# Kernel optimization log

Measured on AMD Instinct MI355X. Metric: run time of the kernel, lower is better.

## Reference

```python
import jax, jax.numpy as jnp
import numpy as np

B, HEADS, T, QH, QW, D = 2, 8, 8, 16, 16, 64
KT, KH, KW = T, QH, QW  # key shape == query shape


def _rel_index(q_n, k_n):
    q_ratio = round(max(k_n / q_n, 1.0))
    k_ratio = round(max(q_n / k_n, 1.0))
    d = jnp.arange(q_n)[:, None] * q_ratio - jnp.arange(k_n)[None, :] * k_ratio
    return d + (k_n - 1) * k_ratio  # [q_n, k_n] indices into embedding table


def setup_inputs() -> dict:
    key = jax.random.key(0)
    k1, k2, k3, k4, k5 = jax.random.split(key, 5)
    query = jax.random.normal(k1, (B, HEADS, T * QH * QW, D), dtype=jnp.float32)
    scores = jax.random.normal(k2, (B, HEADS, T * QH * QW, KT * KH * KW), dtype=jnp.float32)
    height_emb = jax.random.normal(k3, (2 * (max(QH, KH) - 1) + 1, D), dtype=jnp.float32)
    width_emb = jax.random.normal(k4, (2 * (max(QW, KW) - 1) + 1, D), dtype=jnp.float32)
    time_emb = jax.random.normal(k5, (2 * (max(T, KT) - 1) + 1, D), dtype=jnp.float32)
    return {"query": query, "scores": scores, "height_emb": height_emb,
            "width_emb": width_emb, "time_emb": time_emb}


def reference(query, scores, height_emb, width_emb, time_emb):
    # gather relative-position embeddings (static indices)
    Rh = height_emb[_rel_index(QH, KH)]   # [qh, kh, D]
    Rw = width_emb[_rel_index(QW, KW)]    # [qw, kw, D]
    Rt = time_emb[_rel_index(T, KT)]      # [t,  kt, D]

    q = query.reshape(B, HEADS, T, QH, QW, D)
    rel_h = jnp.einsum('bNthwc,hkc->bNthwk', q, Rh)  # [B,N,T,qh,qw,kh]
    rel_w = jnp.einsum('bNthwc,wkc->bNthwk', q, Rw)  # [B,N,T,qh,qw,kw]
    rel_t = jnp.einsum('bNthwc,tkc->bNthwk', q, Rt)  # [B,N,T,qh,qw,kt]

    s = scores.reshape(B, HEADS, T, QH, QW, KT, KH, KW)
    s = s + rel_h[:, :, :, :, :, None, :, None]
    s = s + rel_w[:, :, :, :, :, None, None, :]
    s = s + rel_t[:, :, :, :, :, :, None, None]
    return s.reshape(B, HEADS, T * QH * QW, KT * KH * KW)
```

## Files before the change

kernel.cpp:

```cpp
#include <hip/hip_runtime.h>


__global__ __launch_bounds__(256) void relpos_fused_kernel(
    const float* __restrict__ query,
    const float* __restrict__ scores,
    const float* __restrict__ hemb,
    const float* __restrict__ wemb,
    const float* __restrict__ temb,
    float* __restrict__ out)
{
    __shared__ float q_lds[64];
    __shared__ float relH[16];
    __shared__ float relW[16];
    __shared__ float relT[8];
    __shared__ float relTH[128];

    const int bid = blockIdx.x;
    const int tid = threadIdx.x;
    const int row = bid & 2047;
    const int t   = row >> 8;
    const int qh  = (row >> 4) & 15;
    const int qw  = row & 15;

    if (tid < 16) {
        ((float4*)q_lds)[tid] =
            ((const float4*)(query + (size_t)bid * 64))[tid];
    }
    __syncthreads();

    if (tid < 40) {
        const float* emb;
        int eidx;
        if (tid < 16)      { emb = hemb; eidx = qh - tid + 15; }
        else if (tid < 32) { emb = wemb; eidx = qw - (tid - 16) + 15; }
        else               { emb = temb; eidx = t  - (tid - 32) + 7; }
        const float4* e4 = (const float4*)(emb + eidx * 64);
        const float4* q4p = (const float4*)q_lds;
        float acc = 0.f;
        #pragma unroll
        for (int k = 0; k < 16; ++k) {
            float4 q4 = q4p[k];
            float4 e  = e4[k];
            acc += q4.x * e.x + q4.y * e.y + q4.z * e.z + q4.w * e.w;
        }
        if (tid < 16)      relH[tid] = acc;
        else if (tid < 32) relW[tid - 16] = acc;
        else               relT[tid - 32] = acc;
    }
    __syncthreads();

    if (tid < 128) {
        relTH[tid] = relT[tid >> 4] + relH[tid & 15];
    }
    __syncthreads();

    const size_t base4 = (size_t)bid * 512;
    const float4* s4p = (const float4*)scores + base4;
    float4* o4p = (float4*)out + base4;
    const float4* w4p = (const float4*)relW;

    #pragma unroll
    for (int it = 0; it < 2; ++it) {
        const int j4 = tid + it * 256;
        float4 s = s4p[j4];
        const float a  = relTH[j4 >> 2];
        const float4 w = w4p[j4 & 3];
        float4 o;
        o.x = s.x + a + w.x;
        o.y = s.y + a + w.y;
        o.z = s.z + a + w.z;
        o.w = s.w + a + w.w;
        o4p[j4] = o;
    }
}

extern "C" void kernel_launch(void* const* d_in, const int* in_sizes, int n_in,
                              void* d_out, int out_size, void* d_ws, size_t ws_size,
                              hipStream_t stream) {
    const float* query  = (const float*)d_in[0];
    const float* scores = (const float*)d_in[1];
    const float* hemb   = (const float*)d_in[2];
    const float* wemb   = (const float*)d_in[3];
    const float* temb   = (const float*)d_in[4];
    float* out = (float*)d_out;

    relpos_fused_kernel<<<32768, 256, 0, stream>>>(
        query, scores, hemb, wemb, temb, out);
}
```

Measured before the change: 106.6 us.

## Process four rows per block with per-wave bias computation and nontemporal streaming

Each block now handles four query rows, with each wavefront computing its own row's 40 relative-position dot products directly from global memory. This removes the query LDS staging and the relTH pass, cutting the kernel from three barriers to one. The streaming add uses nontemporal loads and stores over 8 float4 per thread. The grid shrinks by four, which amortizes per-block setup but lowers the block count and puts more bandwidth-bound work on each thread.

```diff
diff --git a/kernel.cpp b/kernel.cpp
--- a/kernel.cpp
+++ b/kernel.cpp
@@ -1,7 +1,11 @@
 #include <hip/hip_runtime.h>
 
 
-__global__ __launch_bounds__(256) void relpos_fused_kernel(
+#define ROWS 4
+
+typedef float v4f __attribute__((ext_vector_type(4)));
+
+__global__ __launch_bounds__(256) void relpos_fused_v3(
     const float* __restrict__ query,
     const float* __restrict__ scores,
     const float* __restrict__ hemb,
@@ -9,68 +13,55 @@
     const float* __restrict__ temb,
     float* __restrict__ out)
 {
-    __shared__ float q_lds[64];
-    __shared__ float relH[16];
-    __shared__ float relW[16];
-    __shared__ float relT[8];
-    __shared__ float relTH[128];
+    __shared__ float biasH[ROWS][16];
+    __shared__ float biasW[ROWS][16];
+    __shared__ float biasT[ROWS][8];
 
-    const int bid = blockIdx.x;
-    const int tid = threadIdx.x;
-    const int row = bid & 2047;
-    const int t   = row >> 8;
-    const int qh  = (row >> 4) & 15;
-    const int qw  = row & 15;
+    const int bid  = blockIdx.x;
+    const int tid  = threadIdx.x;
+    const int wv   = tid >> 6;
+    const int lane = tid & 63;
 
-    if (tid < 16) {
-        ((float4*)q_lds)[tid] =
-            ((const float4*)(query + (size_t)bid * 64))[tid];
+    const int r0   = bid * ROWS;
+    const int row  = (r0 + wv) & 2047;
+    const int t    = row >> 8;
+    const int qh   = (row >> 4) & 15;
+    const int qw   = row & 15;
+
+    if (lane < 40) {
+        const float* emb;
+        int eidx;
+        if (lane < 16)      { emb = hemb; eidx = qh - lane + 15; }
+        else if (lane < 32) { emb = wemb; eidx = qw - (lane - 16) + 15; }
+        else                { emb = temb; eidx = t  - (lane - 32) + 7; }
+        const v4f* e4 = (const v4f*)(emb + eidx * 64);
+        const v4f* q4 = (const v4f*)(query + (size_t)(r0 + wv) * 64);
+        v4f a4 = (v4f)(0.f);
+        #pragma unroll
+        for (int k = 0; k < 16; ++k) {
+            a4 += q4[k] * e4[k];
+        }
+        const float acc = (a4.x + a4.y) + (a4.z + a4.w);
+        if (lane < 16)      biasH[wv][lane] = acc;
+        else if (lane < 32) biasW[wv][lane - 16] = acc;
+        else                biasT[wv][lane - 32] = acc;
     }
     __syncthreads();
 
-    if (tid < 40) {
-        const float* emb;
-        int eidx;
-        if (tid < 16)      { emb = hemb; eidx = qh - tid + 15; }
-        else if (tid < 32) { emb = wemb; eidx = qw - (tid - 16) + 15; }
-        else               { emb = temb; eidx = t  - (tid - 32) + 7; }
-        const float4* e4 = (const float4*)(emb + eidx * 64);
-        const float4* q4p = (const float4*)q_lds;
-        float acc = 0.f;
-        #pragma unroll
-        for (int k = 0; k < 16; ++k) {
-            float4 q4 = q4p[k];
-            float4 e  = e4[k];
-            acc += q4.x * e.x + q4.y * e.y + q4.z * e.z + q4.w * e.w;
-        }
-        if (tid < 16)      relH[tid] = acc;
-        else if (tid < 32) relW[tid - 16] = acc;
-        else               relT[tid - 32] = acc;
-    }
-    __syncthreads();
-
-    if (tid < 128) {
-        relTH[tid] = relT[tid >> 4] + relH[tid & 15];
-    }
-    __syncthreads();
-
-    const size_t base4 = (size_t)bid * 512;
-    const float4* s4p = (const float4*)scores + base4;
-    float4* o4p = (float4*)out + base4;
-    const float4* w4p = (const float4*)relW;
+    const size_t base4 = (size_t)bid * (ROWS * 512);
+    const v4f* s4p = (const v4f*)scores + base4;
+    v4f* o4p = (v4f*)out + base4;
 
     #pragma unroll
-    for (int it = 0; it < 2; ++it) {
-        const int j4 = tid + it * 256;
-        float4 s = s4p[j4];
-        const float a  = relTH[j4 >> 2];
-        const float4 w = w4p[j4 & 3];
-        float4 o;
-        o.x = s.x + a + w.x;
-        o.y = s.y + a + w.y;
-        o.z = s.z + a + w.z;
-        o.w = s.w + a + w.w;
-        o4p[j4] = o;
+    for (int i = 0; i < 2 * ROWS; ++i) {
+        const int idx = tid + i * 256;
+        const int rl  = idx >> 9;
+        const int j   = idx & 511;
+        v4f s = __builtin_nontemporal_load(&s4p[idx]);
+        const float a = biasT[rl][j >> 6] + biasH[rl][(j >> 2) & 15];
+        const v4f w = ((const v4f*)biasW[rl])[j & 3];
+        v4f o = s + a + w;
+        __builtin_nontemporal_store(o, &o4p[idx]);
     }
 }
 
@@ -84,6 +75,6 @@
     const float* temb   = (const float*)d_in[4];
     float* out = (float*)d_out;
 
-    relpos_fused_kernel<<<32768, 256, 0, stream>>>(
+    relpos_fused_v3<<<32768 / ROWS, 256, 0, stream>>>(
         query, scores, hemb, wemb, temb, out);
 }
```

Result: no change. 104.7 us (-1.7%).
